# Optimization experiments

Measured on AMD Instinct MI355X. Metric: run time of the kernel, lower is better.

The kernel has to match this reference:

```python
import jax, jax.numpy as jnp
import numpy as np

N_CLASSES = 3  # hardcoded in the original module (labels == 0/1/2)
EPS = 1e-12    # F.normalize default eps


def setup_inputs() -> dict:
    key = jax.random.key(0)
    k1, k2, k3 = jax.random.split(key, 3)
    query = jax.random.normal(k1, (32768, 256), dtype=jnp.float32)
    memory = jax.random.normal(k2, (3, 512, 256), dtype=jnp.float32)
    labels = jax.random.randint(k3, (32768,), 0, 3, dtype=jnp.int64)
    return {"query": query, "labels": labels, "memory": memory}


def reference(query, labels, memory):
    C, n_cells, d = memory.shape  # (3, 512, 256)
    # ---- read: cross-attention over all C*n_cells memory slots ----
    mem_flat = memory.reshape(C * n_cells, d)
    scores = jax.nn.softmax(query @ mem_flat.T, axis=1)  # (N, C*n_cells)
    q_read = scores @ mem_flat                           # (N, d) == the per-row loop, batched

    # ---- update (training path): masked softmax over queries per class ----
    def upd(c):
        mask = labels == c                               # (N,)
        logits = query @ memory[c].T                     # (N, n_cells)
        logits = jnp.where(mask[:, None], logits, -jnp.inf)
        sq = jax.nn.softmax(logits, axis=0)              # softmax over (masked) queries
        delta = sq.T @ query                             # (n_cells, d); zero rows contribute 0
        new = memory[c] + delta
        norm = jnp.maximum(jnp.linalg.norm(new, axis=1, keepdims=True), EPS)
        return new / norm                                # F.normalize over dim=1

    new_mem = jnp.stack([upd(c) for c in range(C)])      # C is a small fixed constant (3)
    return q_read, jax.lax.stop_gradient(new_mem)        # original detaches updated memory
```

## Files before the change

kernel.cpp:

```cpp
#include <hip/hip_runtime.h>
#include <math.h>

#define NQ    32768
#define DDIM  256
#define NCLS  3
#define CELLS 512
#define STOT  1536
#define BK    32

typedef __attribute__((ext_vector_type(8)))  short bf16x8;
typedef __attribute__((ext_vector_type(16))) float f32x16;

#define ROWF(r) (((r) & 3) + 8 * ((r) >> 2) + 4 * lh)

__device__ __forceinline__ f32x16 mfma16(bf16x8 a, bf16x8 b, f32x16 c) {
    return __builtin_amdgcn_mfma_f32_32x32x16_bf16(a, b, c, 0, 0, 0);
}
__device__ __forceinline__ unsigned short f2bf(float f) {
    const unsigned u = __float_as_uint(f);
    return (unsigned short)((u + 0x7FFFu + ((u >> 16) & 1u)) >> 16);
}
__device__ __forceinline__ float bf2f(unsigned short b) {
    return __uint_as_float(((unsigned)b) << 16);
}
__device__ __forceinline__ void gl16(const unsigned short* g, unsigned short* l) {
    __builtin_amdgcn_global_load_lds(
        (const __attribute__((address_space(1))) unsigned int*)g,
        (__attribute__((address_space(3))) unsigned int*)l, 16, 0, 0);
}

__global__ __launch_bounds__(256) void k_convert(const float* __restrict__ src,
        unsigned short* __restrict__ hi, unsigned short* __restrict__ lo,
        unsigned short* __restrict__ hiT, float* __restrict__ sq, int R) {
    __shared__ unsigned short lh_s[64][65];
    const int r0 = blockIdx.x * 64, k0 = blockIdx.y * 64, t = threadIdx.x;
#pragma unroll
    for (int it = 0; it < 4; ++it) {
        const int idx = t + 256 * it;
        const int rl = idx >> 4, kq = idx & 15;
        const float4 v = *(const float4*)(src + (size_t)(r0 + rl) * DDIM + k0 + kq * 4);
        const unsigned short h0 = f2bf(v.x), h1 = f2bf(v.y), h2 = f2bf(v.z), h3 = f2bf(v.w);
        const unsigned short l0 = f2bf(v.x - bf2f(h0)), l1 = f2bf(v.y - bf2f(h1));
        const unsigned short l2 = f2bf(v.z - bf2f(h2)), l3 = f2bf(v.w - bf2f(h3));
        ushort4 hv; hv.x = h0; hv.y = h1; hv.z = h2; hv.w = h3;
        ushort4 lv; lv.x = l0; lv.y = l1; lv.z = l2; lv.w = l3;
        *(ushort4*)(hi + (size_t)(r0 + rl) * DDIM + k0 + kq * 4) = hv;
        *(ushort4*)(lo + (size_t)(r0 + rl) * DDIM + k0 + kq * 4) = lv;
        lh_s[rl][kq * 4 + 0] = h0; lh_s[rl][kq * 4 + 1] = h1;
        lh_s[rl][kq * 4 + 2] = h2; lh_s[rl][kq * 4 + 3] = h3;
        float ssq = v.x * v.x + v.y * v.y + v.z * v.z + v.w * v.w;
        ssq += __shfl_xor(ssq, 1, 64);
        ssq += __shfl_xor(ssq, 2, 64);
        ssq += __shfl_xor(ssq, 4, 64);
        ssq += __shfl_xor(ssq, 8, 64);
        if (kq == 0) atomicAdd(&sq[r0 + rl], ssq);
    }
    __syncthreads();
#pragma unroll
    for (int it = 0; it < 16; ++it) {
        const int idx = t + 256 * it;
        const int kl = idx >> 6, rl = idx & 63;
        hiT[(size_t)(k0 + kl) * R + r0 + rl] = lh_s[rl][kl];
    }
}

__global__ __launch_bounds__(256) void k_pe(
        const unsigned short* __restrict__ Qhi, const unsigned short* __restrict__ Qlo,
        const unsigned short* __restrict__ Mhi, const unsigned short* __restrict__ Mlo,
        const int* __restrict__ labels, const float* __restrict__ qn2,
        const float* __restrict__ mn2,
        unsigned short* __restrict__ P, unsigned short* __restrict__ ET,
        int ibase, int ch, int ipg) {
    __shared__ unsigned short smem[2][2][2][128][BK];
    typedef unsigned short trt[32][40];
    trt* tr = (trt*)&smem[0][0][0][0][0];

    const int t = threadIdx.x, lane = t & 63, wid = t >> 6;
    const int l31 = lane & 31, lh = lane >> 5;
    const int wi = wid >> 1, wj = wid & 1;
    int ib, jb;
    if (ipg > 0) {
        const int xcd = blockIdx.x & 7, s = blockIdx.x >> 3;
        jb = s % 12; ib = xcd * ipg + s / 12;
    } else { jb = blockIdx.x % 12; ib = blockIdx.x / 12; }
    const int iblk = ib * 128, jblk = jb * 128;
    const int iloc0 = iblk + wi * 64;
    const int j0    = jblk + wj * 64;
    const int cblk  = jb >> 2;

    const int c0 = wid * 128 + lane, c1 = c0 + 64;
    const int r0 = c0 >> 2, o0 = ((c0 & 3) ^ (r0 & 3)) * 8;
    const int r1 = c1 >> 2, o1 = ((c1 & 3) ^ (r1 & 3)) * 8;
    const unsigned short* gA[2] = { Qhi + (size_t)(ibase + iblk) * DDIM,
                                    Qlo + (size_t)(ibase + iblk) * DDIM };
    const unsigned short* gB[2] = { Mhi + (size_t)jblk * DDIM,
                                    Mlo + (size_t)jblk * DDIM };
    auto STAGE = [&](int b, int k0) {
#pragma unroll
        for (int h = 0; h < 2; ++h) {
            gl16(gA[h] + (size_t)r0 * DDIM + k0 + o0, &smem[b][0][h][0][0] + c0 * 8);
            gl16(gA[h] + (size_t)r1 * DDIM + k0 + o1, &smem[b][0][h][0][0] + c1 * 8);
            gl16(gB[h] + (size_t)r0 * DDIM + k0 + o0, &smem[b][1][h][0][0] + c0 * 8);
            gl16(gB[h] + (size_t)r1 * DDIM + k0 + o1, &smem[b][1][h][0][0] + c1 * 8);
        }
    };

    f32x16 acc[2][2] = {};
    const int ra0 = wi * 64 + l31, ra1 = ra0 + 32;
    const int rb0 = wj * 64 + l31, rb1 = rb0 + 32;
    STAGE(0, 0);
    for (int s = 0; s < DDIM / BK; ++s) {
        __syncthreads();
        if (s + 1 < DDIM / BK) STAGE((s + 1) & 1, (s + 1) * BK);
        const int b = s & 1;
#pragma unroll
        for (int t16 = 0; t16 < 2; ++t16) {
            const int oc = t16 * 2 + lh;
            const bf16x8 a0h = *(const bf16x8*)&smem[b][0][0][ra0][(oc ^ (ra0 & 3)) * 8];
            const bf16x8 a1h = *(const bf16x8*)&smem[b][0][0][ra1][(oc ^ (ra1 & 3)) * 8];
            const bf16x8 a0l = *(const bf16x8*)&smem[b][0][1][ra0][(oc ^ (ra0 & 3)) * 8];
            const bf16x8 a1l = *(const bf16x8*)&smem[b][0][1][ra1][(oc ^ (ra1 & 3)) * 8];
            const bf16x8 b0h = *(const bf16x8*)&smem[b][1][0][rb0][(oc ^ (rb0 & 3)) * 8];
            const bf16x8 b1h = *(const bf16x8*)&smem[b][1][0][rb1][(oc ^ (rb1 & 3)) * 8];
            const bf16x8 b0l = *(const bf16x8*)&smem[b][1][1][rb0][(oc ^ (rb0 & 3)) * 8];
            const bf16x8 b1l = *(const bf16x8*)&smem[b][1][1][rb1][(oc ^ (rb1 & 3)) * 8];
            acc[0][0] = mfma16(a0h, b0h, acc[0][0]);
            acc[0][0] = mfma16(a0h, b0l, acc[0][0]);
            acc[0][0] = mfma16(a0l, b0h, acc[0][0]);
            acc[0][1] = mfma16(a0h, b1h, acc[0][1]);
            acc[0][1] = mfma16(a0h, b1l, acc[0][1]);
            acc[0][1] = mfma16(a0l, b1h, acc[0][1]);
            acc[1][0] = mfma16(a1h, b0h, acc[1][0]);
            acc[1][0] = mfma16(a1h, b0l, acc[1][0]);
            acc[1][0] = mfma16(a1l, b0h, acc[1][0]);
            acc[1][1] = mfma16(a1h, b1h, acc[1][1]);
            acc[1][1] = mfma16(a1h, b1l, acc[1][1]);
            acc[1][1] = mfma16(a1l, b1h, acc[1][1]);
        }
    }
    __syncthreads();

#pragma unroll
    for (int ti = 0; ti < 2; ++ti) {
        float qn[16]; unsigned lm = 0;
        const int ig0 = ibase + iloc0 + ti * 32;
#pragma unroll
        for (int r = 0; r < 16; ++r) {
            const int ir = ig0 + ROWF(r);
            qn[r] = 6.0f * sqrtf(qn2[ir]);
            lm |= (unsigned)(labels[ir] == cblk) << r;
        }
#pragma unroll
        for (int tj = 0; tj < 2; ++tj) {
            const int jg = j0 + tj * 32 + l31;
            const float mn = 6.0f * sqrtf(mn2[jg]);
#pragma unroll
            for (int r = 0; r < 16; ++r) {
                const float lg = acc[ti][tj][r];
                const int il = iloc0 + ti * 32 + ROWF(r);
                P[(size_t)il * STOT + jg] = f2bf(__expf(lg - qn[r]));
                const float e = ((lm >> r) & 1u) ? __expf(lg - mn) : 0.0f;
                tr[wid][l31][ROWF(r)] = f2bf(e);
            }
            const int rr = lane >> 1, off = (lane & 1) * 16;
            const unsigned short* lp = &tr[wid][rr][off];
            const bf16x8 w0 = *(const bf16x8*)(lp);
            const bf16x8 w1 = *(const bf16x8*)(lp + 8);
            unsigned short* erow = ET + (size_t)(j0 + tj * 32 + rr) * ch + iloc0 + ti * 32 + off;
            *(bf16x8*)(erow)     = w0;
            *(bf16x8*)(erow + 8) = w1;
        }
    }
}

__global__ __launch_bounds__(256) void k_pv(const unsigned short* __restrict__ P,
        const unsigned short* __restrict__ MhiT,
        float* __restrict__ out, int ibase) {
    __shared__ unsigned short sP[2][64][64];
    __shared__ unsigned short sV[2][128][64];
    const int t = threadIdx.x, lane = t & 63, wid = t >> 6;
    const int l31 = lane & 31, lh = lane >> 5;
    const int wq = wid >> 1, wd = wid & 1;
    const int qblk = blockIdx.x * 64, dblk = blockIdx.y * 128;
    const int d0 = dblk + wd * 64;
    const unsigned short* gP = P + (size_t)qblk * STOT;
    const unsigned short* gV = MhiT + (size_t)dblk * STOT;

    auto STAGE = [&](int b, int k0) {
#pragma unroll
        for (int it = 0; it < 2; ++it) {
            const int c = wid * 128 + it * 64 + lane;
            const int r = c >> 3, o = ((c & 7) ^ (r & 7)) * 8;
            gl16(gP + (size_t)r * STOT + k0 + o, &sP[b][0][0] + c * 8);
        }
#pragma unroll
        for (int it = 0; it < 4; ++it) {
            const int c = wid * 256 + it * 64 + lane;
            const int r = c >> 3, o = ((c & 7) ^ (r & 7)) * 8;
            gl16(gV + (size_t)r * STOT + k0 + o, &sV[b][0][0] + c * 8);
        }
    };

    bf16x8 bones;
    const short ob = (l31 == 0) ? (short)0x3F80 : (short)0;
#pragma unroll
    for (int e = 0; e < 8; ++e) bones[e] = ob;

    f32x16 acc[2] = {};
    f32x16 accS = {};
    const int rp = wq * 32 + l31, rv0 = wd * 64 + l31, rv1 = rv0 + 32;
    STAGE(0, 0);
    for (int s = 0; s < STOT / 64; ++s) {
        __syncthreads();
        if (s + 1 < STOT / 64) STAGE((s + 1) & 1, (s + 1) * 64);
        const int b = s & 1;
#pragma unroll
        for (int t16 = 0; t16 < 4; ++t16) {
            const int oc = t16 * 2 + lh;
            const bf16x8 a0 = *(const bf16x8*)&sP[b][rp][(oc ^ (rp & 7)) * 8];
            const bf16x8 b0 = *(const bf16x8*)&sV[b][rv0][(oc ^ (rv0 & 7)) * 8];
            const bf16x8 b1 = *(const bf16x8*)&sV[b][rv1][(oc ^ (rv1 & 7)) * 8];
            acc[0] = mfma16(a0, b0, acc[0]);
            acc[1] = mfma16(a0, b1, acc[1]);
            accS   = mfma16(a0, bones, accS);
        }
    }
    float rinv[16];
#pragma unroll
    for (int r = 0; r < 16; ++r) rinv[r] = 1.f / __shfl(accS[r], lh << 5, 64);
#pragma unroll
    for (int td = 0; td < 2; ++td) {
#pragma unroll
        for (int r = 0; r < 16; ++r) {
            const int ig = ibase + qblk + wq * 32 + ROWF(r);
            out[(size_t)ig * DDIM + d0 + td * 32 + l31] = acc[td][r] * rinv[r];
        }
    }
}

__global__ __launch_bounds__(256) void k_delta4(const unsigned short* __restrict__ ET,
        const unsigned short* __restrict__ QhiT,
        float* __restrict__ delta, float* __restrict__ colsum,
        int ibase, int ch, int ppx) {
    __shared__ unsigned short sE[2][128][64];
    __shared__ unsigned short sQ[2][128][64];
    const int t = threadIdx.x, lane = t & 63, wid = t >> 6;
    const int l31 = lane & 31, lh = lane >> 5;
    const int wj = wid >> 1, wd = wid & 1;
    int jb, db, kb;
    if (ppx > 0) {
        const int xcd = blockIdx.x & 7, s = blockIdx.x >> 3;
        jb = s % 12;
        const int pidx = xcd * ppx + s / 12;
        kb = pidx >> 1; db = pidx & 1;
    } else {
        jb = blockIdx.x % 12; db = (blockIdx.x / 12) & 1; kb = blockIdx.x / 24;
    }
    const int jblk = jb * 128, dblk = db * 128, i0 = kb * 1024;
    const int j0 = jblk + wj * 64, d0 = dblk + wd * 64;
    const unsigned short* gE = ET + (size_t)jblk * ch + i0;
    const unsigned short* gQ = QhiT + (size_t)dblk * NQ + ibase + i0;

    auto STAGE = [&](int b, int k0) {
#pragma unroll
        for (int it = 0; it < 4; ++it) {
            const int c = wid * 256 + it * 64 + lane;
            const int r = c >> 3, o = ((c & 7) ^ (r & 7)) * 8;
            gl16(gE + (size_t)r * ch + k0 + o, &sE[b][0][0] + c * 8);
            gl16(gQ + (size_t)r * NQ + k0 + o, &sQ[b][0][0] + c * 8);
        }
    };

    bf16x8 bones;
    const short ob = (l31 == 0) ? (short)0x3F80 : (short)0;
#pragma unroll
    for (int e = 0; e < 8; ++e) bones[e] = ob;

    f32x16 acc[2][2] = {};
    f32x16 accS0 = {}, accS1 = {};
    const int re0 = wj * 64 + l31, re1 = re0 + 32;
    const int rq0 = wd * 64 + l31, rq1 = rq0 + 32;
    STAGE(0, 0);
    for (int s = 0; s < 16; ++s) {
        __syncthreads();
        if (s + 1 < 16) STAGE((s + 1) & 1, (s + 1) * 64);
        const int b = s & 1;
#pragma unroll
        for (int t16 = 0; t16 < 4; ++t16) {
            const int oc = t16 * 2 + lh;
            const bf16x8 a0 = *(const bf16x8*)&sE[b][re0][(oc ^ (re0 & 7)) * 8];
            const bf16x8 a1 = *(const bf16x8*)&sE[b][re1][(oc ^ (re1 & 7)) * 8];
            const bf16x8 b0 = *(const bf16x8*)&sQ[b][rq0][(oc ^ (rq0 & 7)) * 8];
            const bf16x8 b1 = *(const bf16x8*)&sQ[b][rq1][(oc ^ (rq1 & 7)) * 8];
            acc[0][0] = mfma16(a0, b0, acc[0][0]);
            acc[0][1] = mfma16(a0, b1, acc[0][1]);
            acc[1][0] = mfma16(a1, b0, acc[1][0]);
            acc[1][1] = mfma16(a1, b1, acc[1][1]);
            if (wd == 0) {
                accS0 = mfma16(a0, bones, accS0);
                accS1 = mfma16(a1, bones, accS1);
            }
        }
    }
#pragma unroll
    for (int tj = 0; tj < 2; ++tj) {
#pragma unroll
        for (int td = 0; td < 2; ++td) {
#pragma unroll
            for (int r = 0; r < 16; ++r) {
                const int jr = j0 + tj * 32 + ROWF(r);
                atomicAdd(&delta[(size_t)jr * DDIM + d0 + td * 32 + l31], acc[tj][td][r]);
            }
        }
    }
    if (wd == 0 && l31 == 0) {
#pragma unroll
        for (int r = 0; r < 16; ++r) {
            atomicAdd(&colsum[j0 + ROWF(r)], accS0[r]);
            atomicAdd(&colsum[j0 + 32 + ROWF(r)], accS1[r]);
        }
    }
}

__global__ void k_final(const float* __restrict__ M,
                        const float* __restrict__ delta,
                        const float* __restrict__ colsum,
                        float* __restrict__ out) {
    const int row  = blockIdx.x * 4 + (threadIdx.x >> 6);
    const int lane = threadIdx.x & 63;
    const float inv = 1.f / colsum[row];
    const float4 mv = *(const float4*)(M + (size_t)row * DDIM + lane * 4);
    const float4 dv = *(const float4*)(delta + (size_t)row * DDIM + lane * 4);
    float4 nv;
    nv.x = fmaf(dv.x, inv, mv.x);
    nv.y = fmaf(dv.y, inv, mv.y);
    nv.z = fmaf(dv.z, inv, mv.z);
    nv.w = fmaf(dv.w, inv, mv.w);
    float ss = nv.x * nv.x + nv.y * nv.y + nv.z * nv.z + nv.w * nv.w;
#pragma unroll
    for (int sh = 1; sh < 64; sh <<= 1) ss += __shfl_xor(ss, sh, 64);
    const float rn = 1.f / fmaxf(sqrtf(ss), 1e-12f);
    nv.x *= rn; nv.y *= rn; nv.z *= rn; nv.w *= rn;
    *(float4*)(out + (size_t)NQ * DDIM + (size_t)row * DDIM + lane * 4) = nv;
}

extern "C" void kernel_launch(void* const* d_in, const int* in_sizes, int n_in,
                              void* d_out, int out_size, void* d_ws, size_t ws_size,
                              hipStream_t stream) {
    const float* Q      = (const float*)d_in[0];
    const int*   labels = (const int*)d_in[1];
    const float* M      = (const float*)d_in[2];
    float* out = (float*)d_out;

    char* p = (char*)d_ws;
    float* colsum = (float*)p;          p += (size_t)STOT * 4;
    float* delta  = (float*)p;          p += (size_t)STOT * DDIM * 4;
    float* qn2    = (float*)p;          p += (size_t)NQ * 4;
    float* mn2    = (float*)p;          p += (size_t)STOT * 4;
    const size_t zero_bytes = (size_t)(p - (char*)d_ws);
    unsigned short* Qhi  = (unsigned short*)p; p += (size_t)NQ * DDIM * 2;
    unsigned short* Qlo  = (unsigned short*)p; p += (size_t)NQ * DDIM * 2;
    unsigned short* QhiT = (unsigned short*)p; p += (size_t)NQ * DDIM * 2;
    unsigned short* Mhi  = (unsigned short*)p; p += (size_t)STOT * DDIM * 2;
    unsigned short* Mlo  = (unsigned short*)p; p += (size_t)STOT * DDIM * 2;
    unsigned short* MhiT = (unsigned short*)p; p += (size_t)STOT * DDIM * 2;
    const size_t fixed_bytes = (size_t)(p - (char*)d_ws);

    int nch = 2;
    while (nch < 32 &&
           fixed_bytes + (size_t)(NQ / nch) * STOT * 2 * 2 > ws_size) nch <<= 1;
    const int ch = NQ / nch;
    unsigned short* Pbuf = (unsigned short*)p;
    unsigned short* ETb  = Pbuf + (size_t)ch * STOT;

    const int ipg    = ((ch / 128) % 8 == 0) ? (ch / 128) / 8 : 0;
    const int ksplit = ch / 1024;
    const int ppx    = ((2 * ksplit) % 8 == 0) ? (2 * ksplit) / 8 : 0;

    hipMemsetAsync(d_ws, 0, zero_bytes, stream);

    k_convert<<<dim3(NQ / 64, 4), 256, 0, stream>>>(Q, Qhi, Qlo, QhiT, qn2, NQ);
    k_convert<<<dim3(STOT / 64, 4), 256, 0, stream>>>(M, Mhi, Mlo, MhiT, mn2, STOT);

    for (int h = 0; h < nch; ++h) {
        const int ibase = h * ch;
        k_pe<<<12 * (ch / 128), 256, 0, stream>>>(Qhi, Qlo, Mhi, Mlo, labels,
                                                  qn2, mn2, Pbuf, ETb, ibase, ch, ipg);
        k_pv<<<dim3(ch / 64, 2), 256, 0, stream>>>(Pbuf, MhiT, out, ibase);
        k_delta4<<<24 * ksplit, 256, 0, stream>>>(ETb, QhiT, delta, colsum,
                                                  ibase, ch, ppx);
    }
    k_final<<<STOT / 4, 256, 0, stream>>>(M, delta, colsum, out);
}
```

Baseline: 303.9 us.

## Use k-group-major LDS layout in GEMM kernels and stage P stores via LDS

Replaces the XOR-swizzled row-major shared-memory tiles in k_pe, k_pv and k_delta4 with a [kgroup][row][8] layout. Each MFMA fragment read is then a contiguous 16-byte access per lane, which should avoid bank conflicts without swizzle arithmetic. Global loads become column-strided per lane group, so coalescing is worse: each lane fetches 16 bytes from a different row. k_pe also transposes the P tile through LDS so it writes 32-byte row chunks instead of scattered 2-byte stores, which should cut uncoalesced global write traffic.

```diff
diff --git a/kernel.cpp b/kernel.cpp
--- a/kernel.cpp
+++ b/kernel.cpp
@@ -71,9 +71,10 @@
         const float* __restrict__ mn2,
         unsigned short* __restrict__ P, unsigned short* __restrict__ ET,
         int ibase, int ch, int ipg) {
-    __shared__ unsigned short smem[2][2][2][128][BK];
+    __shared__ unsigned short smem[2][2][2][4][128][8];
     typedef unsigned short trt[32][40];
-    trt* tr = (trt*)&smem[0][0][0][0][0];
+    trt* trP = (trt*)&smem[0][0][0][0][0][0];
+    trt* trE = trP + 4;
 
     const int t = threadIdx.x, lane = t & 63, wid = t >> 6;
     const int l31 = lane & 31, lh = lane >> 5;
@@ -89,8 +90,7 @@
     const int cblk  = jb >> 2;
 
     const int c0 = wid * 128 + lane, c1 = c0 + 64;
-    const int r0 = c0 >> 2, o0 = ((c0 & 3) ^ (r0 & 3)) * 8;
-    const int r1 = c1 >> 2, o1 = ((c1 & 3) ^ (r1 & 3)) * 8;
+    const int g0 = c0 >> 7, r0 = c0 & 127, g1 = c1 >> 7, r1 = c1 & 127;
     const unsigned short* gA[2] = { Qhi + (size_t)(ibase + iblk) * DDIM,
                                     Qlo + (size_t)(ibase + iblk) * DDIM };
     const unsigned short* gB[2] = { Mhi + (size_t)jblk * DDIM,
@@ -98,10 +98,10 @@
     auto STAGE = [&](int b, int k0) {
 #pragma unroll
         for (int h = 0; h < 2; ++h) {
-            gl16(gA[h] + (size_t)r0 * DDIM + k0 + o0, &smem[b][0][h][0][0] + c0 * 8);
-            gl16(gA[h] + (size_t)r1 * DDIM + k0 + o1, &smem[b][0][h][0][0] + c1 * 8);
-            gl16(gB[h] + (size_t)r0 * DDIM + k0 + o0, &smem[b][1][h][0][0] + c0 * 8);
-            gl16(gB[h] + (size_t)r1 * DDIM + k0 + o1, &smem[b][1][h][0][0] + c1 * 8);
+            gl16(gA[h] + (size_t)r0 * DDIM + k0 + g0 * 8, &smem[b][0][h][0][0][0] + c0 * 8);
+            gl16(gA[h] + (size_t)r1 * DDIM + k0 + g1 * 8, &smem[b][0][h][0][0][0] + c1 * 8);
+            gl16(gB[h] + (size_t)r0 * DDIM + k0 + g0 * 8, &smem[b][1][h][0][0][0] + c0 * 8);
+            gl16(gB[h] + (size_t)r1 * DDIM + k0 + g1 * 8, &smem[b][1][h][0][0][0] + c1 * 8);
         }
     };
 
@@ -116,14 +116,14 @@
 #pragma unroll
         for (int t16 = 0; t16 < 2; ++t16) {
             const int oc = t16 * 2 + lh;
-            const bf16x8 a0h = *(const bf16x8*)&smem[b][0][0][ra0][(oc ^ (ra0 & 3)) * 8];
-            const bf16x8 a1h = *(const bf16x8*)&smem[b][0][0][ra1][(oc ^ (ra1 & 3)) * 8];
-            const bf16x8 a0l = *(const bf16x8*)&smem[b][0][1][ra0][(oc ^ (ra0 & 3)) * 8];
-            const bf16x8 a1l = *(const bf16x8*)&smem[b][0][1][ra1][(oc ^ (ra1 & 3)) * 8];
-            const bf16x8 b0h = *(const bf16x8*)&smem[b][1][0][rb0][(oc ^ (rb0 & 3)) * 8];
-            const bf16x8 b1h = *(const bf16x8*)&smem[b][1][0][rb1][(oc ^ (rb1 & 3)) * 8];
-            const bf16x8 b0l = *(const bf16x8*)&smem[b][1][1][rb0][(oc ^ (rb0 & 3)) * 8];
-            const bf16x8 b1l = *(const bf16x8*)&smem[b][1][1][rb1][(oc ^ (rb1 & 3)) * 8];
+            const bf16x8 a0h = *(const bf16x8*)&smem[b][0][0][oc][ra0][0];
+            const bf16x8 a1h = *(const bf16x8*)&smem[b][0][0][oc][ra1][0];
+            const bf16x8 a0l = *(const bf16x8*)&smem[b][0][1][oc][ra0][0];
+            const bf16x8 a1l = *(const bf16x8*)&smem[b][0][1][oc][ra1][0];
+            const bf16x8 b0h = *(const bf16x8*)&smem[b][1][0][oc][rb0][0];
+            const bf16x8 b1h = *(const bf16x8*)&smem[b][1][0][oc][rb1][0];
+            const bf16x8 b0l = *(const bf16x8*)&smem[b][1][1][oc][rb0][0];
+            const bf16x8 b1l = *(const bf16x8*)&smem[b][1][1][oc][rb1][0];
             acc[0][0] = mfma16(a0h, b0h, acc[0][0]);
             acc[0][0] = mfma16(a0h, b0l, acc[0][0]);
             acc[0][0] = mfma16(a0l, b0h, acc[0][0]);
@@ -157,18 +157,29 @@
 #pragma unroll
             for (int r = 0; r < 16; ++r) {
                 const float lg = acc[ti][tj][r];
-                const int il = iloc0 + ti * 32 + ROWF(r);
-                P[(size_t)il * STOT + jg] = f2bf(__expf(lg - qn[r]));
+                trP[wid][ROWF(r)][l31] = f2bf(__expf(lg - qn[r]));
                 const float e = ((lm >> r) & 1u) ? __expf(lg - mn) : 0.0f;
-                tr[wid][l31][ROWF(r)] = f2bf(e);
+                trE[wid][l31][ROWF(r)] = f2bf(e);
             }
             const int rr = lane >> 1, off = (lane & 1) * 16;
-            const unsigned short* lp = &tr[wid][rr][off];
-            const bf16x8 w0 = *(const bf16x8*)(lp);
-            const bf16x8 w1 = *(const bf16x8*)(lp + 8);
-            unsigned short* erow = ET + (size_t)(j0 + tj * 32 + rr) * ch + iloc0 + ti * 32 + off;
-            *(bf16x8*)(erow)     = w0;
-            *(bf16x8*)(erow + 8) = w1;
+            {
+                const unsigned short* lp = &trP[wid][rr][off];
+                const bf16x8 w0 = *(const bf16x8*)(lp);
+                const bf16x8 w1 = *(const bf16x8*)(lp + 8);
+                unsigned short* prow = P + (size_t)(iloc0 + ti * 32 + rr) * STOT
+                                         + j0 + tj * 32 + off;
+                *(bf16x8*)(prow)     = w0;
+                *(bf16x8*)(prow + 8) = w1;
+            }
+            {
+                const unsigned short* lp = &trE[wid][rr][off];
+                const bf16x8 w0 = *(const bf16x8*)(lp);
+                const bf16x8 w1 = *(const bf16x8*)(lp + 8);
+                unsigned short* erow = ET + (size_t)(j0 + tj * 32 + rr) * ch
+                                          + iloc0 + ti * 32 + off;
+                *(bf16x8*)(erow)     = w0;
+                *(bf16x8*)(erow + 8) = w1;
+            }
         }
     }
 }
@@ -176,8 +187,8 @@
 __global__ __launch_bounds__(256) void k_pv(const unsigned short* __restrict__ P,
         const unsigned short* __restrict__ MhiT,
         float* __restrict__ out, int ibase) {
-    __shared__ unsigned short sP[2][64][64];
-    __shared__ unsigned short sV[2][128][64];
+    __shared__ unsigned short sP[2][8][64][8];
+    __shared__ unsigned short sV[2][8][128][8];
     const int t = threadIdx.x, lane = t & 63, wid = t >> 6;
     const int l31 = lane & 31, lh = lane >> 5;
     const int wq = wid >> 1, wd = wid & 1;
@@ -190,14 +201,14 @@
 #pragma unroll
         for (int it = 0; it < 2; ++it) {
             const int c = wid * 128 + it * 64 + lane;
-            const int r = c >> 3, o = ((c & 7) ^ (r & 7)) * 8;
-            gl16(gP + (size_t)r * STOT + k0 + o, &sP[b][0][0] + c * 8);
+            const int g = c >> 6, r = c & 63;
+            gl16(gP + (size_t)r * STOT + k0 + g * 8, &sP[b][0][0][0] + c * 8);
         }
 #pragma unroll
         for (int it = 0; it < 4; ++it) {
             const int c = wid * 256 + it * 64 + lane;
-            const int r = c >> 3, o = ((c & 7) ^ (r & 7)) * 8;
-            gl16(gV + (size_t)r * STOT + k0 + o, &sV[b][0][0] + c * 8);
+            const int g = c >> 7, r = c & 127;
+            gl16(gV + (size_t)r * STOT + k0 + g * 8, &sV[b][0][0][0] + c * 8);
         }
     };
 
@@ -217,9 +228,9 @@
 #pragma unroll
         for (int t16 = 0; t16 < 4; ++t16) {
             const int oc = t16 * 2 + lh;
-            const bf16x8 a0 = *(const bf16x8*)&sP[b][rp][(oc ^ (rp & 7)) * 8];
-            const bf16x8 b0 = *(const bf16x8*)&sV[b][rv0][(oc ^ (rv0 & 7)) * 8];
-            const bf16x8 b1 = *(const bf16x8*)&sV[b][rv1][(oc ^ (rv1 & 7)) * 8];
+            const bf16x8 a0 = *(const bf16x8*)&sP[b][oc][rp][0];
+            const bf16x8 b0 = *(const bf16x8*)&sV[b][oc][rv0][0];
+            const bf16x8 b1 = *(const bf16x8*)&sV[b][oc][rv1][0];
             acc[0] = mfma16(a0, b0, acc[0]);
             acc[1] = mfma16(a0, b1, acc[1]);
             accS   = mfma16(a0, bones, accS);
@@ -242,8 +253,8 @@
         const unsigned short* __restrict__ QhiT,
         float* __restrict__ delta, float* __restrict__ colsum,
         int ibase, int ch, int ppx) {
-    __shared__ unsigned short sE[2][128][64];
-    __shared__ unsigned short sQ[2][128][64];
+    __shared__ unsigned short sE[2][8][128][8];
+    __shared__ unsigned short sQ[2][8][128][8];
     const int t = threadIdx.x, lane = t & 63, wid = t >> 6;
     const int l31 = lane & 31, lh = lane >> 5;
     const int wj = wid >> 1, wd = wid & 1;
@@ -265,9 +276,9 @@
 #pragma unroll
         for (int it = 0; it < 4; ++it) {
             const int c = wid * 256 + it * 64 + lane;
-            const int r = c >> 3, o = ((c & 7) ^ (r & 7)) * 8;
-            gl16(gE + (size_t)r * ch + k0 + o, &sE[b][0][0] + c * 8);
-            gl16(gQ + (size_t)r * NQ + k0 + o, &sQ[b][0][0] + c * 8);
+            const int g = c >> 7, r = c & 127;
+            gl16(gE + (size_t)r * ch + k0 + g * 8, &sE[b][0][0][0] + c * 8);
+            gl16(gQ + (size_t)r * NQ + k0 + g * 8, &sQ[b][0][0][0] + c * 8);
         }
     };
 
@@ -288,10 +299,10 @@
 #pragma unroll
         for (int t16 = 0; t16 < 4; ++t16) {
             const int oc = t16 * 2 + lh;
-            const bf16x8 a0 = *(const bf16x8*)&sE[b][re0][(oc ^ (re0 & 7)) * 8];
-            const bf16x8 a1 = *(const bf16x8*)&sE[b][re1][(oc ^ (re1 & 7)) * 8];
-            const bf16x8 b0 = *(const bf16x8*)&sQ[b][rq0][(oc ^ (rq0 & 7)) * 8];
-            const bf16x8 b1 = *(const bf16x8*)&sQ[b][rq1][(oc ^ (rq1 & 7)) * 8];
+            const bf16x8 a0 = *(const bf16x8*)&sE[b][oc][re0][0];
+            const bf16x8 a1 = *(const bf16x8*)&sE[b][oc][re1][0];
+            const bf16x8 b0 = *(const bf16x8*)&sQ[b][oc][rq0][0];
+            const bf16x8 b1 = *(const bf16x8*)&sQ[b][oc][rq1][0];
             acc[0][0] = mfma16(a0, b0, acc[0][0]);
             acc[0][1] = mfma16(a0, b1, acc[0][1]);
             acc[1][0] = mfma16(a1, b0, acc[1][0]);
```

New measurement: 366.2 us. 20.5% more time.

## Use 512-thread k_pe blocks with 64x32 warp tiles and allow single-chunk processing

Applied to the files above, without the earlier changes.

k_pe now runs 8 waves per block instead of 4. Each wave computes a 64x32 tile instead of 64x64, which halves its accumulators and cuts register pressure. LDS staging is split into separate A and B buffers, each thread issues one load per operand, and the swizzle is changed to suit the new read pattern. The chunk loop now starts at nch=1, so when the workspace is large enough all queries are processed in one pass with fewer launches. The cost is more A-operand LDS reads per MFMA, plus larger P/E buffers that may fall out of cache between kernels.

```diff
diff --git a/kernel.cpp b/kernel.cpp
--- a/kernel.cpp
+++ b/kernel.cpp
@@ -64,20 +64,21 @@
     }
 }
 
-__global__ __launch_bounds__(256) void k_pe(
+__global__ __launch_bounds__(512) void k_pe(
         const unsigned short* __restrict__ Qhi, const unsigned short* __restrict__ Qlo,
         const unsigned short* __restrict__ Mhi, const unsigned short* __restrict__ Mlo,
         const int* __restrict__ labels, const float* __restrict__ qn2,
         const float* __restrict__ mn2,
         unsigned short* __restrict__ P, unsigned short* __restrict__ ET,
         int ibase, int ch, int ipg) {
-    __shared__ unsigned short smem[2][2][2][128][BK];
+    __shared__ unsigned short sA[2][2][128][BK];
+    __shared__ unsigned short sB[2][2][128][BK];
     typedef unsigned short trt[32][40];
-    trt* tr = (trt*)&smem[0][0][0][0][0];
+    trt* trE = (trt*)&sA[0][0][0][0];
 
     const int t = threadIdx.x, lane = t & 63, wid = t >> 6;
     const int l31 = lane & 31, lh = lane >> 5;
-    const int wi = wid >> 1, wj = wid & 1;
+    const int wi = wid >> 2, wj = wid & 3;
     int ib, jb;
     if (ipg > 0) {
         const int xcd = blockIdx.x & 7, s = blockIdx.x >> 3;
@@ -85,12 +86,10 @@
     } else { jb = blockIdx.x % 12; ib = blockIdx.x / 12; }
     const int iblk = ib * 128, jblk = jb * 128;
     const int iloc0 = iblk + wi * 64;
-    const int j0    = jblk + wj * 64;
+    const int j0    = jblk + wj * 32;
     const int cblk  = jb >> 2;
 
-    const int c0 = wid * 128 + lane, c1 = c0 + 64;
-    const int r0 = c0 >> 2, o0 = ((c0 & 3) ^ (r0 & 3)) * 8;
-    const int r1 = c1 >> 2, o1 = ((c1 & 3) ^ (r1 & 3)) * 8;
+    const int cA = t, rA = cA >> 2, oA = ((cA ^ (cA >> 3)) & 3) * 8;
     const unsigned short* gA[2] = { Qhi + (size_t)(ibase + iblk) * DDIM,
                                     Qlo + (size_t)(ibase + iblk) * DDIM };
     const unsigned short* gB[2] = { Mhi + (size_t)jblk * DDIM,
@@ -98,16 +97,16 @@
     auto STAGE = [&](int b, int k0) {
 #pragma unroll
         for (int h = 0; h < 2; ++h) {
-            gl16(gA[h] + (size_t)r0 * DDIM + k0 + o0, &smem[b][0][h][0][0] + c0 * 8);
-            gl16(gA[h] + (size_t)r1 * DDIM + k0 + o1, &smem[b][0][h][0][0] + c1 * 8);
-            gl16(gB[h] + (size_t)r0 * DDIM + k0 + o0, &smem[b][1][h][0][0] + c0 * 8);
-            gl16(gB[h] + (size_t)r1 * DDIM + k0 + o1, &smem[b][1][h][0][0] + c1 * 8);
+            gl16(gA[h] + (size_t)rA * DDIM + k0 + oA, &sA[b][h][0][0] + cA * 8);
+            gl16(gB[h] + (size_t)rA * DDIM + k0 + oA, &sB[b][h][0][0] + cA * 8);
         }
     };
 
-    f32x16 acc[2][2] = {};
+    f32x16 acc[2] = {};
     const int ra0 = wi * 64 + l31, ra1 = ra0 + 32;
-    const int rb0 = wj * 64 + l31, rb1 = rb0 + 32;
+    const int rb  = wj * 32 + l31;
+    const int swa = (ra0 >> 1) & 3;
+    const int swb = (rb >> 1) & 3;
     STAGE(0, 0);
     for (int s = 0; s < DDIM / BK; ++s) {
         __syncthreads();
@@ -116,30 +115,25 @@
 #pragma unroll
         for (int t16 = 0; t16 < 2; ++t16) {
             const int oc = t16 * 2 + lh;
-            const bf16x8 a0h = *(const bf16x8*)&smem[b][0][0][ra0][(oc ^ (ra0 & 3)) * 8];
-            const bf16x8 a1h = *(const bf16x8*)&smem[b][0][0][ra1][(oc ^ (ra1 & 3)) * 8];
-            const bf16x8 a0l = *(const bf16x8*)&smem[b][0][1][ra0][(oc ^ (ra0 & 3)) * 8];
-            const bf16x8 a1l = *(const bf16x8*)&smem[b][0][1][ra1][(oc ^ (ra1 & 3)) * 8];
-            const bf16x8 b0h = *(const bf16x8*)&smem[b][1][0][rb0][(oc ^ (rb0 & 3)) * 8];
-            const bf16x8 b1h = *(const bf16x8*)&smem[b][1][0][rb1][(oc ^ (rb1 & 3)) * 8];
-            const bf16x8 b0l = *(const bf16x8*)&smem[b][1][1][rb0][(oc ^ (rb0 & 3)) * 8];
-            const bf16x8 b1l = *(const bf16x8*)&smem[b][1][1][rb1][(oc ^ (rb1 & 3)) * 8];
-            acc[0][0] = mfma16(a0h, b0h, acc[0][0]);
-            acc[0][0] = mfma16(a0h, b0l, acc[0][0]);
-            acc[0][0] = mfma16(a0l, b0h, acc[0][0]);
-            acc[0][1] = mfma16(a0h, b1h, acc[0][1]);
-            acc[0][1] = mfma16(a0h, b1l, acc[0][1]);
-            acc[0][1] = mfma16(a0l, b1h, acc[0][1]);
-            acc[1][0] = mfma16(a1h, b0h, acc[1][0]);
-            acc[1][0] = mfma16(a1h, b0l, acc[1][0]);
-            acc[1][0] = mfma16(a1l, b0h, acc[1][0]);
-            acc[1][1] = mfma16(a1h, b1h, acc[1][1]);
-            acc[1][1] = mfma16(a1h, b1l, acc[1][1]);
-            acc[1][1] = mfma16(a1l, b1h, acc[1][1]);
+            const int ka = (oc ^ swa) * 8, kb = (oc ^ swb) * 8;
+            const bf16x8 a0h = *(const bf16x8*)&sA[b][0][ra0][ka];
+            const bf16x8 a1h = *(const bf16x8*)&sA[b][0][ra1][ka];
+            const bf16x8 a0l = *(const bf16x8*)&sA[b][1][ra0][ka];
+            const bf16x8 a1l = *(const bf16x8*)&sA[b][1][ra1][ka];
+            const bf16x8 b0h = *(const bf16x8*)&sB[b][0][rb][kb];
+            const bf16x8 b0l = *(const bf16x8*)&sB[b][1][rb][kb];
+            acc[0] = mfma16(a0h, b0h, acc[0]);
+            acc[0] = mfma16(a0h, b0l, acc[0]);
+            acc[0] = mfma16(a0l, b0h, acc[0]);
+            acc[1] = mfma16(a1h, b0h, acc[1]);
+            acc[1] = mfma16(a1h, b0l, acc[1]);
+            acc[1] = mfma16(a1l, b0h, acc[1]);
         }
     }
     __syncthreads();
 
+    const int jg = j0 + l31;
+    const float mn = 6.0f * sqrtf(mn2[jg]);
 #pragma unroll
     for (int ti = 0; ti < 2; ++ti) {
         float qn[16]; unsigned lm = 0;
@@ -151,25 +145,20 @@
             lm |= (unsigned)(labels[ir] == cblk) << r;
         }
 #pragma unroll
-        for (int tj = 0; tj < 2; ++tj) {
-            const int jg = j0 + tj * 32 + l31;
-            const float mn = 6.0f * sqrtf(mn2[jg]);
-#pragma unroll
-            for (int r = 0; r < 16; ++r) {
-                const float lg = acc[ti][tj][r];
-                const int il = iloc0 + ti * 32 + ROWF(r);
-                P[(size_t)il * STOT + jg] = f2bf(__expf(lg - qn[r]));
-                const float e = ((lm >> r) & 1u) ? __expf(lg - mn) : 0.0f;
-                tr[wid][l31][ROWF(r)] = f2bf(e);
-            }
-            const int rr = lane >> 1, off = (lane & 1) * 16;
-            const unsigned short* lp = &tr[wid][rr][off];
-            const bf16x8 w0 = *(const bf16x8*)(lp);
-            const bf16x8 w1 = *(const bf16x8*)(lp + 8);
-            unsigned short* erow = ET + (size_t)(j0 + tj * 32 + rr) * ch + iloc0 + ti * 32 + off;
-            *(bf16x8*)(erow)     = w0;
-            *(bf16x8*)(erow + 8) = w1;
-        }
+        for (int r = 0; r < 16; ++r) {
+            const float lg = acc[ti][r];
+            P[(size_t)(iloc0 + ti * 32 + ROWF(r)) * STOT + jg]
+                = f2bf(__expf(lg - qn[r]));
+            const float e = ((lm >> r) & 1u) ? __expf(lg - mn) : 0.0f;
+            trE[wid][l31][ROWF(r)] = f2bf(e);
+        }
+        const int rr = lane >> 1, off = (lane & 1) * 16;
+        const unsigned short* lp = &trE[wid][rr][off];
+        const bf16x8 w0 = *(const bf16x8*)(lp);
+        const bf16x8 w1 = *(const bf16x8*)(lp + 8);
+        unsigned short* erow = ET + (size_t)(j0 + rr) * ch + iloc0 + ti * 32 + off;
+        *(bf16x8*)(erow)     = w0;
+        *(bf16x8*)(erow + 8) = w1;
     }
 }
 
@@ -366,7 +355,7 @@
     unsigned short* MhiT = (unsigned short*)p; p += (size_t)STOT * DDIM * 2;
     const size_t fixed_bytes = (size_t)(p - (char*)d_ws);
 
-    int nch = 2;
+    int nch = 1;
     while (nch < 32 &&
            fixed_bytes + (size_t)(NQ / nch) * STOT * 2 * 2 > ws_size) nch <<= 1;
     const int ch = NQ / nch;
@@ -384,7 +373,7 @@
 
     for (int h = 0; h < nch; ++h) {
         const int ibase = h * ch;
-        k_pe<<<12 * (ch / 128), 256, 0, stream>>>(Qhi, Qlo, Mhi, Mlo, labels,
+        k_pe<<<12 * (ch / 128), 512, 0, stream>>>(Qhi, Qlo, Mhi, Mlo, labels,
                                                   qn2, mn2, Pbuf, ETb, ibase, ch, ipg);
         k_pv<<<dim3(ch / 64, 2), 256, 0, stream>>>(Pbuf, MhiT, out, ibase);
         k_delta4<<<24 * ksplit, 256, 0, stream>>>(ETb, QhiT, delta, colsum,
```

New measurement: 316.4 us. 4.1% more time.
